# Kernel optimization log

Measured on AMD Instinct MI355X. Metric: run time of the kernel, lower is better.

## Reference

```python
import jax, jax.numpy as jnp
import numpy as np

C = 1  # channels (depthwise conv group count)
N_ITER = 10
EPS = 1e-12


def _dwconv(x, w):
    # depthwise valid conv, NCHW input, OIHW weight with O=C, I=1
    return jax.lax.conv_general_dilated(
        x, w, window_strides=(1, 1), padding='VALID',
        dimension_numbers=('NCHW', 'OIHW', 'NCHW'), feature_group_count=C)


def _forward_grad(u, f_grad, f_grad2):
    gx = _dwconv(jnp.pad(u, ((0, 0), (0, 0), (0, 0), (0, 1))), f_grad)
    gx = gx.at[:, :, :, -1].set(0.0)
    gy = _dwconv(jnp.pad(u, ((0, 0), (0, 0), (0, 1), (0, 0))), f_grad2)
    gy = gy.at[:, :, -1, :].set(0.0)
    return gx, gy


def _divergence(px, py, div_w, div_w2):
    tx = jnp.pad(px[:, :, :, :-1], ((0, 0), (0, 0), (0, 0), (1, 0)))
    ty = jnp.pad(py[:, :, :-1, :], ((0, 0), (0, 0), (1, 0), (0, 0)))
    gx = _dwconv(jnp.pad(tx, ((0, 0), (0, 0), (0, 0), (0, 1))), div_w)
    gy = _dwconv(jnp.pad(ty, ((0, 0), (0, 0), (0, 1), (0, 0))), div_w2)
    return gx + gy


def setup_inputs() -> dict:
    key = jax.random.key(0)
    k1, k2 = jax.random.split(key)
    B, H, W = 64, 256, 256
    x = jax.random.normal(k1, (B, C, H, W), dtype=jnp.float32)
    y = jax.random.normal(k2, (B, C, H, W), dtype=jnp.float32)
    img_grad = jnp.tile(jnp.array([[[[-0.5, 0.0, 0.5]]]], jnp.float32), (C, 1, 1, 1))   # (C,1,1,3)
    img_grad2 = jnp.tile(jnp.array([[[[-0.5], [0.0], [0.5]]]], jnp.float32), (C, 1, 1, 1))  # (C,1,3,1)
    f_grad = jnp.tile(jnp.array([[[[-1.0, 1.0]]]], jnp.float32), (C, 1, 1, 1))          # (C,1,1,2)
    f_grad2 = jnp.tile(jnp.array([[[[-1.0], [1.0]]]], jnp.float32), (C, 1, 1, 1))       # (C,1,2,1)
    div_w = jnp.tile(jnp.array([[[[-1.0, 1.0]]]], jnp.float32), (C, 1, 1, 1))
    div_w2 = jnp.tile(jnp.array([[[[-1.0], [1.0]]]], jnp.float32), (C, 1, 1, 1))
    t = jnp.array([0.3], jnp.float32)
    l = jnp.array([0.15], jnp.float32)
    a = jnp.array([0.25], jnp.float32)
    return {'x': x, 'y': y, 'img_grad': img_grad, 'img_grad2': img_grad2,
            'f_grad': f_grad, 'f_grad2': f_grad2, 'div_w': div_w, 'div_w2': div_w2,
            't': t, 'l': l, 'a': a}


def reference(x, y, img_grad, img_grad2, f_grad, f_grad2, div_w, div_w2, t, l, a):
    l_t = (l * t)[0]
    taut = (a / t)[0]
    ts = t[0]

    # centered image gradients of y with replicated boundary corrections from x
    g2x = _dwconv(jnp.pad(y, ((0, 0), (0, 0), (0, 0), (1, 1))), img_grad)
    g2x = g2x.at[:, :, :, 0].set(0.5 * (x[:, :, :, 1] - x[:, :, :, 0]))
    g2x = g2x.at[:, :, :, -1].set(0.5 * (x[:, :, :, -1] - x[:, :, :, -2]))
    g2y = _dwconv(jnp.pad(y, ((0, 0), (0, 0), (1, 1), (0, 0))), img_grad2)
    g2y = g2y.at[:, :, 0, :].set(0.5 * (x[:, :, 1, :] - x[:, :, 0, :]))
    g2y = g2y.at[:, :, -1, :].set(0.5 * (x[:, :, -1, :] - x[:, :, -2, :]))

    grad = g2x * g2x + g2y * g2y + EPS
    u1 = jnp.zeros_like(x)
    u2 = jnp.zeros_like(x)
    rho_c = y - g2x * u1 - g2y * u2 - x  # u1=u2=0 initially
    p11 = jnp.zeros_like(x); p12 = jnp.zeros_like(x)
    p21 = jnp.zeros_like(x); p22 = jnp.zeros_like(x)

    zero = jnp.zeros_like(x)
    for _ in range(N_ITER):
        rho = rho_c + g2x * u1 + g2y * u2 + EPS
        mask1 = rho < -l_t * grad
        mask2 = rho > l_t * grad
        mask3 = (~mask1) & (~mask2) & (grad > EPS)
        s = -rho / grad
        v1 = jnp.where(mask1, l_t * g2x, jnp.where(mask2, -l_t * g2x, jnp.where(mask3, s * g2x, zero)))
        v2 = jnp.where(mask1, l_t * g2y, jnp.where(mask2, -l_t * g2y, jnp.where(mask3, s * g2y, zero)))
        v1 = v1 + u1
        v2 = v2 + u2
        u1 = v1 + ts * _divergence(p11, p12, div_w, div_w2)
        u2 = v2 + ts * _divergence(p21, p22, div_w, div_w2)
        u1x, u1y = _forward_grad(u1, f_grad, f_grad2)
        u2x, u2y = _forward_grad(u2, f_grad, f_grad2)
        n1 = jnp.sqrt(u1x * u1x + u1y * u1y + EPS)
        n2 = jnp.sqrt(u2x * u2x + u2y * u2y + EPS)
        p11 = (p11 + taut * u1x) / (1.0 + taut * n1)
        p12 = (p12 + taut * u1y) / (1.0 + taut * n1)
        p21 = (p21 + taut * u2x) / (1.0 + taut * n2)
        p22 = (p22 + taut * u2y) / (1.0 + taut * n2)
    return (u1, u2)
```

## Files before the change

### kernel.cpp

```cpp
#include <hip/hip_runtime.h>
#include <hip/hip_fp16.h>

#define HH 256
#define WW 256
#define NB 64
#define NPIX (NB * HH * WW)
#define NF4  (NPIX / 4)
#define ROW4 (WW / 4)
#define EPSF 1e-12f
#define NTHR 256
#define NBLK (NF4 / NTHR)
#define FTRH 16
#define FTHR 1024
#define FBLK (NB * (HH / FTRH))
#define NIT  3
#define NU   (FTRH + 2 * NIT)
#define NPR  (FTRH + 2 * NIT - 1)

__device__ __forceinline__ float4 ld4(const float* p, int f) {
    return ((const float4*)p)[f];
}
__device__ __forceinline__ void st4(float* p, int f, const float* v) {
    ((float4*)p)[f] = make_float4(v[0], v[1], v[2], v[3]);
}
__device__ __forceinline__ void ld8h(const __half2* p, int f, float* a, float* b) {
    float4 raw = ((const float4*)p)[f];
    const __half2* h = (const __half2*)&raw;
    #pragma unroll
    for (int k = 0; k < 4; ++k) {
        float2 v = __half22float2(h[k]);
        a[k] = v.x; b[k] = v.y;
    }
}
__device__ __forceinline__ void st8h(__half2* p, int f, const float* a, const float* b) {
    float4 raw;
    __half2* h = (__half2*)&raw;
    #pragma unroll
    for (int k = 0; k < 4; ++k) h[k] = __floats2half2_rn(a[k], b[k]);
    ((float4*)p)[f] = raw;
}
__device__ __forceinline__ float4 pack4h2(const float* a, const float* b) {
    float4 raw;
    __half2* h = (__half2*)&raw;
    #pragma unroll
    for (int k = 0; k < 4; ++k) h[k] = __floats2half2_rn(a[k], b[k]);
    return raw;
}
__device__ __forceinline__ void unpack4h2(float4 raw, float* a, float* b) {
    const __half2* h = (const __half2*)&raw;
    #pragma unroll
    for (int k = 0; k < 4; ++k) {
        float2 v = __half22float2(h[k]);
        a[k] = v.x; b[k] = v.y;
    }
}

__device__ __forceinline__ void thresh(
    float gx, float gy, float rho, float grad, float l_t,
    float& v1, float& v2)
{
    float s = -rho * __builtin_amdgcn_rcpf(grad);
    float c = __builtin_amdgcn_fmed3f(s, -l_t, l_t);
    v1 = c * gx; v2 = c * gy;
}

__device__ __forceinline__ void pupd(
    float pao, float pbo, float ux, float uy, float taut,
    float& pa, float& pb)
{
    float n2 = fmaf(ux, ux, fmaf(uy, uy, EPSF));
    float n  = __builtin_amdgcn_sqrtf(n2);
    float r  = __builtin_amdgcn_rcpf(fmaf(taut, n, 1.f));
    pa = fmaf(taut, ux, pao) * r;
    pb = fmaf(taut, uy, pbo) * r;
}

__global__ __launch_bounds__(NTHR) void s_kernel(
    const float* __restrict__ x, const float* __restrict__ y,
    __half2* __restrict__ ga, float* __restrict__ rc)
{
    int f = blockIdx.x * NTHR + threadIdx.x;
    int idx = f << 2;
    int i  = (idx >> 8) & 255;
    int j0 = idx & 255;

    float4 xc4 = ld4(x, f), yc4 = ld4(y, f);
    const float* xc = (const float*)&xc4;
    const float* yc = (const float*)&yc4;

    float4 a4, b4;
    if (i == 0)            { a4 = ld4(x, f + ROW4); b4 = xc4; }
    else if (i == HH - 1)  { a4 = xc4; b4 = ld4(x, f - ROW4); }
    else                   { a4 = ld4(y, f + ROW4); b4 = ld4(y, f - ROW4); }
    const float* aa = (const float*)&a4;
    const float* bb = (const float*)&b4;

    float yl = (j0 > 0)      ? y[idx - 1] : 0.f;
    float yr = (j0 < WW - 4) ? y[idx + 4] : 0.f;

    float gxo[4], gyo[4], rco[4];
    #pragma unroll
    for (int k = 0; k < 4; ++k) {
        int j = j0 + k;
        float gx;
        if (j == 0)            gx = 0.5f * (xc[1] - xc[0]);
        else if (j == WW - 1)  gx = 0.5f * (xc[3] - xc[2]);
        else {
            float ynext = (k < 3) ? yc[k + 1] : yr;
            float yprev = (k > 0) ? yc[k - 1] : yl;
            gx = 0.5f * (ynext - yprev);
        }
        float gy = 0.5f * (aa[k] - bb[k]);
        gxo[k] = gx; gyo[k] = gy;
        rco[k] = yc[k] - xc[k];
    }
    st8h(ga, f, gxo, gyo); st4(rc, f, rco);
}

template <bool P0, bool LAST>
__global__ __launch_bounds__(FTHR) void fp_kernel(
    const __half2* __restrict__ ga, const float* __restrict__ rc,
    const __half2* __restrict__ upi,
    const __half2* __restrict__ pai, const __half2* __restrict__ pbi,
    __half2* __restrict__ upo,
    float* __restrict__ u1f, float* __restrict__ u2f,
    __half2* __restrict__ pao, __half2* __restrict__ pbo,
    const float* __restrict__ tp, const float* __restrict__ lp,
    const float* __restrict__ ap)
{
    __shared__ alignas(16) __half2 sU [NU ][WW];
    __shared__ alignas(16) __half2 sPA[NPR][WW];
    __shared__ alignas(16) __half2 sPB[NPR][WW];

    const float ts   = tp[0];
    const float l_t  = lp[0] * ts;
    const float taut = ap[0] / ts;

    const int t     = threadIdx.x;
    const int tile  = blockIdx.x;
    const int i0    = (tile & 15) * FTRH;
    const int base4 = (tile >> 4) * (HH * ROW4);

    const int tr  = t >> 6;
    const int tcg = t & 63;
    const int tc  = tcg * 4;

    for (int rr = tr - NIT; rr <= FTRH + NIT - 1; rr += FTRH) {
        int gr = i0 + rr;
        float4* dst = (float4*)&sU[rr + NIT][tc];
        if (gr >= 0 && gr < HH) {
            int f = base4 + gr * ROW4 + tcg;
            if (P0) {
                float gx[4], gy[4];
                ld8h(ga, f, gx, gy);
                float4 rc4 = ld4(rc, f);
                const float* rcv = (const float*)&rc4;
                float v1[4], v2[4];
                #pragma unroll
                for (int k = 0; k < 4; ++k) {
                    float grad = fmaf(gx[k], gx[k], fmaf(gy[k], gy[k], EPSF));
                    float rho  = rcv[k] + EPSF;
                    thresh(gx[k], gy[k], rho, grad, l_t, v1[k], v2[k]);
                }
                *dst = pack4h2(v1, v2);
            } else {
                *dst = ((const float4*)upi)[f];
            }
        } else {
            *dst = make_float4(0.f, 0.f, 0.f, 0.f);
        }
    }
    __syncthreads();

    #pragma unroll
    for (int m = 0; m < NIT; ++m) {
        const int plo = -(NIT - m);
        const int phi = FTRH - 1 + (NIT - 1 - m);
        for (int rr = tr + plo; rr <= phi; rr += FTRH) {
            int gr = i0 + rr;
            int li = rr + NIT;
            if (gr >= 0 && gr < HH) {
                float u1c[4], u2c[4];
                float u1d[4] = {0,0,0,0}, u2d[4] = {0,0,0,0};
                unpack4h2(*(const float4*)&sU[li][tc], u1c, u2c);
                bool hasDn = (gr < HH - 1);
                if (hasDn) unpack4h2(*(const float4*)&sU[li + 1][tc], u1d, u2d);
                float u1r = 0.f, u2r = 0.f;
                if (tc < WW - 4) {
                    float2 v = __half22float2(sU[li][tc + 4]);
                    u1r = v.x; u2r = v.y;
                }
                float c11[4], c12[4], c21[4], c22[4];
                if (m == 0) {
                    if (P0) {
                        #pragma unroll
                        for (int k = 0; k < 4; ++k) { c11[k]=c12[k]=c21[k]=c22[k]=0.f; }
                    } else {
                        int f = base4 + gr * ROW4 + tcg;
                        ld8h(pai, f, c11, c12);
                        ld8h(pbi, f, c21, c22);
                    }
                } else {
                    unpack4h2(*(const float4*)&sPA[li][tc], c11, c21);
                    unpack4h2(*(const float4*)&sPB[li][tc], c12, c22);
                }
                float p11n[4], p12n[4], p21n[4], p22n[4];
                #pragma unroll
                for (int k = 0; k < 4; ++k) {
                    int j = tc + k;
                    float du1 = (k < 3) ? u1c[k + 1] : u1r;
                    float du2 = (k < 3) ? u2c[k + 1] : u2r;
                    float u1x = (j < WW - 1) ? du1 - u1c[k] : 0.f;
                    float u2x = (j < WW - 1) ? du2 - u2c[k] : 0.f;
                    float u1y = hasDn ? u1d[k] - u1c[k] : 0.f;
                    float u2y = hasDn ? u2d[k] - u2c[k] : 0.f;
                    pupd(c11[k], c12[k], u1x, u1y, taut, p11n[k], p12n[k]);
                    pupd(c21[k], c22[k], u2x, u2y, taut, p21n[k], p22n[k]);
                }
                *(float4*)&sPA[li][tc] = pack4h2(p11n, p21n);
                *(float4*)&sPB[li][tc] = pack4h2(p12n, p22n);
                if (m == NIT - 1 && !LAST && rr >= 0 && rr < FTRH) {
                    int f = base4 + gr * ROW4 + tcg;
                    st8h(pao, f, p11n, p12n);
                    st8h(pbo, f, p21n, p22n);
                }
            } else {
                *(float4*)&sPA[li][tc] = make_float4(0.f, 0.f, 0.f, 0.f);
                *(float4*)&sPB[li][tc] = make_float4(0.f, 0.f, 0.f, 0.f);
            }
        }
        __syncthreads();

        const int ulo = -(NIT - 1 - m);
        const int uhi = FTRH - 1 + (NIT - 1 - m);
        for (int rr = tr + ulo; rr <= uhi; rr += FTRH) {
            int gr = i0 + rr;
            int li = rr + NIT;
            if (gr < 0 || gr >= HH) continue;
            int f = base4 + gr * ROW4 + tcg;
            float gx[4], gy[4];
            ld8h(ga, f, gx, gy);
            float4 rc4 = ld4(rc, f);
            const float* rcv = (const float*)&rc4;
            float u1c[4], u2c[4];
            unpack4h2(*(const float4*)&sU[li][tc], u1c, u2c);
            float p11[4], p21[4], p12[4], p22[4], q12[4], q22[4];
            unpack4h2(*(const float4*)&sPA[li][tc], p11, p21);
            unpack4h2(*(const float4*)&sPB[li][tc], p12, p22);
            unpack4h2(*(const float4*)&sPB[li - 1][tc], q12, q22);
            float l11 = 0.f, l21 = 0.f;
            if (tc > 0) {
                float2 lv = __half22float2(sPA[li][tc - 1]);
                l11 = lv.x; l21 = lv.y;
            }
            bool hasDn = (gr < HH - 1);
            float u1n[4], u2n[4];
            #pragma unroll
            for (int k = 0; k < 4; ++k) {
                int j = tc + k;
                float t11  = (j < WW - 1) ? p11[k] : 0.f;
                float t21  = (j < WW - 1) ? p21[k] : 0.f;
                float l11k = (k == 0) ? l11 : p11[k - 1];
                float l21k = (k == 0) ? l21 : p21[k - 1];
                float t12  = hasDn ? p12[k] : 0.f;
                float t22  = hasDn ? p22[k] : 0.f;
                float div1 = (t11 - l11k) + (t12 - q12[k]);
                float div2 = (t21 - l21k) + (t22 - q22[k]);

                float grad = fmaf(gx[k], gx[k], fmaf(gy[k], gy[k], EPSF));
                float rho  = rcv[k] + gx[k]*u1c[k] + gy[k]*u2c[k] + EPSF;
                float v1, v2;
                thresh(gx[k], gy[k], rho, grad, l_t, v1, v2);
                u1n[k] = v1 + u1c[k] + ts * div1;
                u2n[k] = v2 + u2c[k] + ts * div2;
            }
            if (m == NIT - 1) {
                if (LAST) { st4(u1f, f, u1n); st4(u2f, f, u2n); }
                else      { st8h(upo, f, u1n, u2n); }
            } else {
                *(float4*)&sU[li][tc] = pack4h2(u1n, u2n);
            }
        }
        if (m < NIT - 1) __syncthreads();
    }
}

extern "C" void kernel_launch(void* const* d_in, const int* in_sizes, int n_in,
                              void* d_out, int out_size, void* d_ws, size_t ws_size,
                              hipStream_t stream) {
    const float* x = (const float*)d_in[0];
    const float* y = (const float*)d_in[1];
    const float* t = (const float*)d_in[8];
    const float* l = (const float*)d_in[9];
    const float* a = (const float*)d_in[10];

    float* u1out = (float*)d_out;
    float* u2out = u1out + NPIX;

    char* ws = (char*)d_ws;
    float*   rcp_ = (float*)ws;                              ws += (size_t)NPIX * 4;
    __half2* gaP  = (__half2*)ws;                            ws += (size_t)NPIX * 4;
    __half2* upA  = (__half2*)ws;                            ws += (size_t)NPIX * 4;
    __half2* upB  = (__half2*)ws;                            ws += (size_t)NPIX * 4;
    __half2* paA  = (__half2*)ws;                            ws += (size_t)NPIX * 4;
    __half2* pbA  = (__half2*)ws;                            ws += (size_t)NPIX * 4;
    __half2* paB  = (__half2*)ws;                            ws += (size_t)NPIX * 4;
    __half2* pbB  = (__half2*)ws;

    s_kernel<<<dim3(NBLK), dim3(NTHR), 0, stream>>>(x, y, gaP, rcp_);

    fp_kernel<true, false><<<dim3(FBLK), dim3(FTHR), 0, stream>>>(
        gaP, rcp_, nullptr, nullptr, nullptr,
        upA, nullptr, nullptr, paA, pbA, t, l, a);

    fp_kernel<false, false><<<dim3(FBLK), dim3(FTHR), 0, stream>>>(
        gaP, rcp_, upA, paA, pbA,
        upB, nullptr, nullptr, paB, pbB, t, l, a);

    fp_kernel<false, true><<<dim3(FBLK), dim3(FTHR), 0, stream>>>(
        gaP, rcp_, upB, paB, pbB,
        nullptr, u1out, u2out, nullptr, nullptr, t, l, a);
}
```

Baseline: 236.7 us.

## Halve fused tile height and use wave shuffles for neighbor column values

Shrinks the fused multi-iteration tile from 16 to 8 rows, using 512-thread blocks with a min-blocks launch bound of 8, to cut LDS per block and raise occupancy. Horizontal neighbor values that were fetched from global memory or LDS are now exchanged between adjacent lanes of a 64-wide wavefront with __shfl_up/__shfl_down. The cost is that the 3-iteration row halo becomes much larger relative to the tile, so more rows are recomputed per block. The aggressive launch bound may also force register pressure or spills.

```diff
diff --git a/kernel.cpp b/kernel.cpp
--- a/kernel.cpp
+++ b/kernel.cpp
@@ -10,9 +10,10 @@
 #define EPSF 1e-12f
 #define NTHR 256
 #define NBLK (NF4 / NTHR)
-#define FTRH 16
-#define FTHR 1024
-#define FBLK (NB * (HH / FTRH))
+#define FTRH 8
+#define FTHR 512
+#define TPI  (HH / FTRH)
+#define FBLK (NB * TPI)
 #define NIT  3
 #define NU   (FTRH + 2 * NIT)
 #define NPR  (FTRH + 2 * NIT - 1)
@@ -53,6 +54,11 @@
         float2 v = __half22float2(h[k]);
         a[k] = v.x; b[k] = v.y;
     }
+}
+__device__ __forceinline__ void h2w(unsigned int w, float& a, float& b) {
+    __half2 h = *(__half2*)&w;
+    float2 v = __half22float2(h);
+    a = v.x; b = v.y;
 }
 
 __device__ __forceinline__ void thresh(
@@ -82,7 +88,6 @@
     int f = blockIdx.x * NTHR + threadIdx.x;
     int idx = f << 2;
     int i  = (idx >> 8) & 255;
-    int j0 = idx & 255;
 
     float4 xc4 = ld4(x, f), yc4 = ld4(y, f);
     const float* xc = (const float*)&xc4;
@@ -95,9 +100,10 @@
     const float* aa = (const float*)&a4;
     const float* bb = (const float*)&b4;
 
-    float yl = (j0 > 0)      ? y[idx - 1] : 0.f;
-    float yr = (j0 < WW - 4) ? y[idx + 4] : 0.f;
-
+    float yl = __shfl_up(yc4.w, 1);
+    float yr = __shfl_down(yc4.x, 1);
+
+    int j0 = idx & 255;
     float gxo[4], gyo[4], rco[4];
     #pragma unroll
     for (int k = 0; k < 4; ++k) {
@@ -118,7 +124,7 @@
 }
 
 template <bool P0, bool LAST>
-__global__ __launch_bounds__(FTHR) void fp_kernel(
+__global__ __launch_bounds__(FTHR, 8) void fp_kernel(
     const __half2* __restrict__ ga, const float* __restrict__ rc,
     const __half2* __restrict__ upi,
     const __half2* __restrict__ pai, const __half2* __restrict__ pbi,
@@ -138,8 +144,8 @@
 
     const int t     = threadIdx.x;
     const int tile  = blockIdx.x;
-    const int i0    = (tile & 15) * FTRH;
-    const int base4 = (tile >> 4) * (HH * ROW4);
+    const int i0    = (tile & (TPI - 1)) * FTRH;
+    const int base4 = (tile / TPI) * (HH * ROW4);
 
     const int tr  = t >> 6;
     const int tcg = t & 63;
@@ -180,16 +186,15 @@
             int gr = i0 + rr;
             int li = rr + NIT;
             if (gr >= 0 && gr < HH) {
+                float4 rawU = *(const float4*)&sU[li][tc];
                 float u1c[4], u2c[4];
+                unpack4h2(rawU, u1c, u2c);
                 float u1d[4] = {0,0,0,0}, u2d[4] = {0,0,0,0};
-                unpack4h2(*(const float4*)&sU[li][tc], u1c, u2c);
                 bool hasDn = (gr < HH - 1);
                 if (hasDn) unpack4h2(*(const float4*)&sU[li + 1][tc], u1d, u2d);
-                float u1r = 0.f, u2r = 0.f;
-                if (tc < WW - 4) {
-                    float2 v = __half22float2(sU[li][tc + 4]);
-                    u1r = v.x; u2r = v.y;
-                }
+                unsigned int w0 = ((const unsigned int*)&rawU)[0];
+                unsigned int nb = __shfl_down((int)w0, 1);
+                float u1r, u2r;  h2w(nb, u1r, u2r);
                 float c11[4], c12[4], c21[4], c22[4];
                 if (m == 0) {
                     if (P0) {
@@ -244,15 +249,15 @@
             const float* rcv = (const float*)&rc4;
             float u1c[4], u2c[4];
             unpack4h2(*(const float4*)&sU[li][tc], u1c, u2c);
+            float4 rawA = *(const float4*)&sPA[li][tc];
             float p11[4], p21[4], p12[4], p22[4], q12[4], q22[4];
-            unpack4h2(*(const float4*)&sPA[li][tc], p11, p21);
+            unpack4h2(rawA, p11, p21);
             unpack4h2(*(const float4*)&sPB[li][tc], p12, p22);
             unpack4h2(*(const float4*)&sPB[li - 1][tc], q12, q22);
-            float l11 = 0.f, l21 = 0.f;
-            if (tc > 0) {
-                float2 lv = __half22float2(sPA[li][tc - 1]);
-                l11 = lv.x; l21 = lv.y;
-            }
+            unsigned int w3 = ((const unsigned int*)&rawA)[3];
+            unsigned int lw = __shfl_up((int)w3, 1);
+            float l11, l21;  h2w(lw, l11, l21);
+            if (tcg == 0) { l11 = 0.f; l21 = 0.f; }
             bool hasDn = (gr < HH - 1);
             float u1n[4], u2n[4];
             #pragma unroll
```

Result: faster. 226.8 us (-4.2%).
